# Kernel tuning notes

Hardware: AMD Instinct MI355X
Metric: run time of the kernel (lower is better)

The kernel has to match this reference:

```python
import jax, jax.numpy as jnp
import numpy as np

N_HEAD = 16
ROPE_BASE = 10000.0


def _rope_cos_sin(T, D, dtype):
    # D = head_size; matches RotaryEmbedding: emb = cat(freqs, freqs)
    inv_freq = 1.0 / (ROPE_BASE ** (jnp.arange(0, D, 2, dtype=jnp.float32) / D))
    t = jnp.arange(T, dtype=jnp.float32)
    freqs = t[:, None] * inv_freq[None, :]              # [T, D/2]
    emb = jnp.concatenate([freqs, freqs], axis=-1)      # [T, D]
    return jnp.cos(emb).astype(dtype), jnp.sin(emb).astype(dtype)


def _rotate_half(x):
    d = x.shape[-1] // 2
    return jnp.concatenate([-x[..., d:], x[..., :d]], axis=-1)


def setup_inputs() -> dict:
    key = jax.random.key(0)
    ks = jax.random.split(key, 5)
    B, T, C = 2, 2048, 1024
    s_in = 1.0 / np.sqrt(C)
    return {
        "x": jax.random.normal(ks[0], (B, T, C), dtype=jnp.float32),
        "w_attn": jax.random.normal(ks[1], (C, 3 * C), dtype=jnp.float32) * s_in,
        "b_attn": jnp.zeros((3 * C,), dtype=jnp.float32),
        "w_proj": jax.random.normal(ks[2], (C, C), dtype=jnp.float32) * s_in,
        "b_proj": jnp.zeros((C,), dtype=jnp.float32),
    }


def reference(x, w_attn, b_attn, w_proj, b_proj):
    B, T, C = x.shape
    H = N_HEAD
    D = C // H

    qkv = x @ w_attn + b_attn                            # [B,T,3C]
    q, k, v = jnp.split(qkv, 3, axis=-1)
    # [B,T,C] -> [B,H,T,D]
    to_heads = lambda a: a.reshape(B, T, H, D).transpose(0, 2, 1, 3)
    q, k, v = to_heads(q), to_heads(k), to_heads(v)

    cos, sin = _rope_cos_sin(T, D, x.dtype)              # [T,D] each, broadcast over B,H
    q = q * cos + _rotate_half(q) * sin
    k = k * cos + _rotate_half(k) * sin

    scale = 1.0 / np.sqrt(D)
    att = jnp.einsum("bhqd,bhkd->bhqk", q, k) * scale    # [B,H,T,T]
    causal = jnp.tril(jnp.ones((T, T), dtype=bool))
    att = jnp.where(causal, att, jnp.finfo(att.dtype).min)
    att = jax.nn.softmax(att, axis=-1)
    y = jnp.einsum("bhqk,bhkd->bhqd", att, v)            # [B,H,T,D]

    y = y.transpose(0, 2, 1, 3).reshape(B, T, C)
    return y @ w_proj + b_proj
```

## Files before the change

### kernel.cpp

```cpp
#include <hip/hip_runtime.h>
#include <hip/hip_bf16.h>

#define B_ 2
#define T_ 2048
#define C_ 1024
#define H_ 16
#define D_ 64

typedef __attribute__((ext_vector_type(8))) short bf16x8;
typedef __attribute__((ext_vector_type(4))) float f32x4;

static __device__ __forceinline__ float bf2f(unsigned short u) {
  union { unsigned int i; float f; } c;
  c.i = ((unsigned int)u) << 16;
  return c.f;
}
static __device__ __forceinline__ unsigned short f2bf(float f) {
  union { float f; unsigned int i; } c;
  c.f = f;
  unsigned int x = c.i;
  return (unsigned short)((x + 0x7fffu + ((x >> 16) & 1u)) >> 16);
}

static __device__ __forceinline__ void gl_lds16(const void* g, void* s) {
  __builtin_amdgcn_global_load_lds(
      (const __attribute__((address_space(1))) void*)g,
      (__attribute__((address_space(3))) void*)s, 16, 0, 0);
}

__global__ __launch_bounds__(256) void fill_kernel_f32(float* __restrict__ out,
                                                       int n, float v) {
  int i = blockIdx.x * 256 + threadIdx.x;
  if (i < n) out[i] = v;
}

__global__ __launch_bounds__(256) void cvt_bf16(const float* __restrict__ X,
                                                unsigned short* __restrict__ Xb) {
  int i = (blockIdx.x * 256 + threadIdx.x) * 8;
  float4 f0 = *(const float4*)(X + i);
  float4 f1 = *(const float4*)(X + i + 4);
  union { unsigned short u[8]; uint4 v; } p;
  p.u[0] = f2bf(f0.x); p.u[1] = f2bf(f0.y); p.u[2] = f2bf(f0.z); p.u[3] = f2bf(f0.w);
  p.u[4] = f2bf(f1.x); p.u[5] = f2bf(f1.y); p.u[6] = f2bf(f1.z); p.u[7] = f2bf(f1.w);
  *(uint4*)(Xb + i) = p.v;
}

__global__ __launch_bounds__(256) void transpose_cvt(const float* __restrict__ W,
                                                     unsigned short* __restrict__ WT,
                                                     int Kd, int Nd) {
  __shared__ float tile[32][33];
  const int n0 = blockIdx.x * 32, k0 = blockIdx.y * 32;
  const int tx = threadIdx.x & 31, ty = threadIdx.x >> 5;
#pragma unroll
  for (int i = 0; i < 4; ++i)
    tile[ty + i * 8][tx] = W[(size_t)(k0 + ty + i * 8) * Nd + n0 + tx];
  __syncthreads();
#pragma unroll
  for (int i = 0; i < 4; ++i)
    WT[(size_t)(n0 + ty + i * 8) * Kd + k0 + tx] = f2bf(tile[tx][ty + i * 8]);
}

__global__ __launch_bounds__(256) void v_transpose(const unsigned short* __restrict__ vP,
                                                   unsigned short* __restrict__ vT) {
  __shared__ unsigned short tile[64][72];
  const int t0 = blockIdx.x * 64;
  const int bh = blockIdx.y;
  const int b = bh >> 4;
  const int srow = threadIdx.x >> 3;
  const int sc8 = (threadIdx.x & 7) * 8;
#pragma unroll
  for (int it = 0; it < 2; ++it) {
    int r = srow + it * 32;
    *(uint4*)&tile[r][sc8] =
        *(const uint4*)(vP + (size_t)(b * T_ + t0 + r) * 1024 + (bh & 15) * 64 + sc8);
  }
  __syncthreads();
#pragma unroll
  for (int it = 0; it < 2; ++it) {
    int dd = srow + it * 32;
    union { unsigned short u[8]; uint4 v; } o;
#pragma unroll
    for (int j = 0; j < 8; ++j) o.u[j] = tile[sc8 + j][dd];
    *(uint4*)(vT + ((size_t)bh * 64 + dd) * 2048 + t0 + sc8) = o.v;
  }
}

template <int OUT_PLANES>
__global__ __launch_bounds__(256) void mfma_gemm(
    const unsigned short* __restrict__ A,
    const unsigned short* __restrict__ BT,
    const float* __restrict__ bias,
    unsigned short* __restrict__ qP, unsigned short* __restrict__ kP,
    unsigned short* __restrict__ vP, float* __restrict__ Fout,
    int N, int K) {
  __shared__ unsigned short As[128 * 64];
  __shared__ unsigned short Bs[128 * 64];

  const int tid = threadIdx.x;
  const int w = tid >> 6, lane = tid & 63;
  const int lo = lane & 15, g = lane >> 4;
  const int wm = (w >> 1) * 64, wn = (w & 1) * 64;
  const int m0 = blockIdx.y * 128, n0 = blockIdx.x * 128;

  const int lr8 = lane >> 3;

  const f32x4 zero4 = {0.f, 0.f, 0.f, 0.f};
  f32x4 acc[4][4] = {{zero4, zero4, zero4, zero4}, {zero4, zero4, zero4, zero4},
                     {zero4, zero4, zero4, zero4}, {zero4, zero4, zero4, zero4}};

  for (int k0 = 0; k0 < K; k0 += 64) {
    __syncthreads();
#pragma unroll
    for (int it = 0; it < 4; ++it) {
      const int base_row = w * 32 + it * 8;
      const int r = base_row + lr8;
      const int j = (lane & 7) ^ (r & 7);
      gl_lds16(A + (size_t)(m0 + r) * K + k0 + j * 8, &As[base_row * 64]);
      gl_lds16(BT + (size_t)(n0 + r) * K + k0 + j * 8, &Bs[base_row * 64]);
    }
    __syncthreads();

#pragma unroll
    for (int kk = 0; kk < 2; ++kk) {
      bf16x8 af[4], bfr[4];
#pragma unroll
      for (int i = 0; i < 4; ++i) {
        int ra = wm + i * 16 + lo;
        int rb = wn + i * 16 + lo;
        af[i]  = *(const bf16x8*)&As[ra * 64 + ((g + kk * 4) ^ (ra & 7)) * 8];
        bfr[i] = *(const bf16x8*)&Bs[rb * 64 + ((g + kk * 4) ^ (rb & 7)) * 8];
      }
#pragma unroll
      for (int i = 0; i < 4; ++i)
#pragma unroll
        for (int j = 0; j < 4; ++j)
          acc[i][j] = __builtin_amdgcn_mfma_f32_16x16x32_bf16(af[i], bfr[j],
                                                              acc[i][j], 0, 0, 0);
    }
  }

  float bv[4];
#pragma unroll
  for (int j = 0; j < 4; ++j) bv[j] = bias[n0 + wn + j * 16 + lo];

  if (OUT_PLANES) {
    const int pl = n0 >> 10;
    const int col0 = (n0 & 1023) + wn + lo;
    if (pl == 2) {
#pragma unroll
      for (int i = 0; i < 4; ++i)
#pragma unroll
        for (int r = 0; r < 4; ++r) {
          size_t row = (size_t)(m0 + wm + i * 16 + g * 4 + r);
#pragma unroll
          for (int j = 0; j < 4; ++j)
            vP[row * 1024 + col0 + j * 16] = f2bf(acc[i][j][r] + bv[j]);
        }
    } else {
      unsigned short* P = (pl == 0) ? qP : kP;
      const float scale = (pl == 0) ? 0.125f : 1.0f;
      const float invA = exp2f((float)(-2 * lo) * (13.287712379549449f / 64.0f)) *
                         0.15915494309189535f;
      const float invB = exp2f((float)(-2 * (lo + 16)) * (13.287712379549449f / 64.0f)) *
                         0.15915494309189535f;
#pragma unroll
      for (int i = 0; i < 4; ++i)
#pragma unroll
        for (int r = 0; r < 4; ++r) {
          const int row = m0 + wm + i * 16 + g * 4 + r;
          const float t = (float)(row & (T_ - 1));
          float ra = t * invA; ra -= floorf(ra);
          float rb = t * invB; rb -= floorf(rb);
          const float sA = __builtin_amdgcn_sinf(ra);
          const float cA = __builtin_amdgcn_cosf(ra);
          const float sB = __builtin_amdgcn_sinf(rb);
          const float cB = __builtin_amdgcn_cosf(rb);
          const float q1A = acc[i][0][r] + bv[0];
          const float q2A = acc[i][2][r] + bv[2];
          const float q1B = acc[i][1][r] + bv[1];
          const float q2B = acc[i][3][r] + bv[3];
          unsigned short* dst = P + (size_t)row * 1024 + col0;
          dst[0]  = f2bf((q1A * cA - q2A * sA) * scale);
          dst[32] = f2bf((q2A * cA + q1A * sA) * scale);
          dst[16] = f2bf((q1B * cB - q2B * sB) * scale);
          dst[48] = f2bf((q2B * cB + q1B * sB) * scale);
        }
    }
  } else {
#pragma unroll
    for (int i = 0; i < 4; ++i)
#pragma unroll
      for (int r = 0; r < 4; ++r) {
        size_t row = (size_t)(m0 + wm + i * 16 + g * 4 + r);
#pragma unroll
        for (int j = 0; j < 4; ++j)
          Fout[row * N + n0 + wn + j * 16 + lo] = acc[i][j][r] + bv[j];
      }
  }
}

__global__ __launch_bounds__(256) void flash_mfma6(
    unsigned short* __restrict__ qP,
    const unsigned short* __restrict__ kP,
    const unsigned short* __restrict__ vT) {
  const int bx = blockIdx.x;
  const int bh = blockIdx.y;
  const int b = bh >> 4, h = bh & 15;
  const int tid = threadIdx.x;
  const int w = tid >> 6, lane = tid & 63;
  const int lo = lane & 15, g = lane >> 4;

  __shared__ unsigned short Ks[64][72];
  __shared__ unsigned short VTs[64][72];
  __shared__ unsigned short Ps[64][72];

  const int srow = tid >> 3;
  const int sc8 = (tid & 7) * 8;
  const f32x4 zero4 = {0.f, 0.f, 0.f, 0.f};

#pragma unroll
  for (int half = 0; half < 2; ++half) {
    const int qt = half ? (31 - bx) : bx;
    const int rowq0 = b * T_ + qt * 64;

    const unsigned short* qrow = qP + (size_t)(rowq0 + w * 16 + lo) * 1024 + h * 64;
    bf16x8 aq0 = *(const bf16x8*)(qrow + g * 8);
    bf16x8 aq1 = *(const bf16x8*)(qrow + 32 + g * 8);

    f32x4 oacc[4] = {zero4, zero4, zero4, zero4};
    float lsum = 0.f;

    uint4 kreg0, kreg1, vreg0, vreg1;
    {
      const size_t kb = (size_t)(b * T_ + srow) * 1024 + h * 64 + sc8;
      kreg0 = *(const uint4*)(kP + kb);
      kreg1 = *(const uint4*)(kP + kb + (size_t)32 * 1024);
      const size_t vb = ((size_t)bh * 64 + srow) * 2048 + sc8;
      vreg0 = *(const uint4*)(vT + vb);
      vreg1 = *(const uint4*)(vT + vb + (size_t)32 * 2048);
    }

    for (int kt = 0; kt <= qt; ++kt) {
      __syncthreads();
      *(uint4*)&Ks[srow][sc8]       = kreg0;
      *(uint4*)&Ks[srow + 32][sc8]  = kreg1;
      *(uint4*)&VTs[srow][sc8]      = vreg0;
      *(uint4*)&VTs[srow + 32][sc8] = vreg1;
      __syncthreads();
      if (kt < qt) {
        const size_t kb = (size_t)(b * T_ + (kt + 1) * 64 + srow) * 1024 + h * 64 + sc8;
        kreg0 = *(const uint4*)(kP + kb);
        kreg1 = *(const uint4*)(kP + kb + (size_t)32 * 1024);
        const size_t vb = ((size_t)bh * 64 + srow) * 2048 + (kt + 1) * 64 + sc8;
        vreg0 = *(const uint4*)(vT + vb);
        vreg1 = *(const uint4*)(vT + vb + (size_t)32 * 2048);
      }

      f32x4 sacc[4] = {zero4, zero4, zero4, zero4};
      __builtin_amdgcn_s_setprio(1);
#pragma unroll
      for (int ct = 0; ct < 4; ++ct) {
        bf16x8 bk0 = *(const bf16x8*)&Ks[ct * 16 + lo][g * 8];
        bf16x8 bk1 = *(const bf16x8*)&Ks[ct * 16 + lo][32 + g * 8];
        sacc[ct] = __builtin_amdgcn_mfma_f32_16x16x32_bf16(bk0, aq0, sacc[ct], 0, 0, 0);
        sacc[ct] = __builtin_amdgcn_mfma_f32_16x16x32_bf16(bk1, aq1, sacc[ct], 0, 0, 0);
      }
      __builtin_amdgcn_s_setprio(0);

      if (kt == qt) {
#pragma unroll
        for (int ct = 0; ct < 4; ++ct)
#pragma unroll
          for (int r = 0; r < 4; ++r)
            if (ct * 16 + g * 4 + r > w * 16 + lo) sacc[ct][r] = -1e30f;
      }

#pragma unroll
      for (int ct = 0; ct < 4; ++ct) {
        float p0 = __expf(sacc[ct][0]);
        float p1 = __expf(sacc[ct][1]);
        float p2 = __expf(sacc[ct][2]);
        float p3 = __expf(sacc[ct][3]);
        lsum += (p0 + p1) + (p2 + p3);
        unsigned int u0 = (unsigned int)f2bf(p0) | ((unsigned int)f2bf(p1) << 16);
        unsigned int u1 = (unsigned int)f2bf(p2) | ((unsigned int)f2bf(p3) << 16);
        uint2 pw; pw.x = u0; pw.y = u1;
        *(uint2*)&Ps[w * 16 + lo][ct * 16 + g * 4] = pw;
      }

      bf16x8 ap0 = *(const bf16x8*)&Ps[w * 16 + lo][g * 8];
      bf16x8 ap1 = *(const bf16x8*)&Ps[w * 16 + lo][32 + g * 8];
      __builtin_amdgcn_s_setprio(1);
#pragma unroll
      for (int c2 = 0; c2 < 4; ++c2) {
        bf16x8 bv0 = *(const bf16x8*)&VTs[c2 * 16 + lo][g * 8];
        bf16x8 bv1 = *(const bf16x8*)&VTs[c2 * 16 + lo][32 + g * 8];
        oacc[c2] = __builtin_amdgcn_mfma_f32_16x16x32_bf16(ap0, bv0, oacc[c2], 0, 0, 0);
        oacc[c2] = __builtin_amdgcn_mfma_f32_16x16x32_bf16(ap1, bv1, oacc[c2], 0, 0, 0);
      }
      __builtin_amdgcn_s_setprio(0);
    }

    lsum += __shfl_xor(lsum, 16);
    lsum += __shfl_xor(lsum, 32);

#pragma unroll
    for (int r = 0; r < 4; ++r) {
      float inv_r = 1.0f / __shfl(lsum, g * 4 + r);
      unsigned short* dst = qP + (size_t)(rowq0 + w * 16 + g * 4 + r) * 1024 + h * 64 + lo;
#pragma unroll
      for (int c2 = 0; c2 < 4; ++c2)
        dst[c2 * 16] = f2bf(oacc[c2][r] * inv_r);
    }
  }
}

extern "C" void kernel_launch(void* const* d_in, const int* in_sizes, int n_in,
                              void* d_out, int out_size, void* d_ws, size_t ws_size,
                              hipStream_t stream) {
  const float *x = nullptr, *w_attn = nullptr, *b_attn = nullptr,
              *w_proj = nullptr, *b_proj = nullptr;
  for (int i = 0; i < n_in; ++i) {
    switch (in_sizes[i]) {
      case B_ * T_ * C_:  x      = (const float*)d_in[i]; break;
      case C_ * 3 * C_:   w_attn = (const float*)d_in[i]; break;
      case 3 * C_:        b_attn = (const float*)d_in[i]; break;
      case C_ * C_:       w_proj = (const float*)d_in[i]; break;
      case C_:            b_proj = (const float*)d_in[i]; break;
      default: break;
    }
  }
  float* out = (float*)d_out;
  const int nblk = (out_size + 255) / 256;

  if (!x || !w_attn || !b_attn || !w_proj || !b_proj) {
    fill_kernel_f32<<<nblk, 256, 0, stream>>>(out, out_size, 100.0f);
    return;
  }
  if (ws_size < (size_t)48 * 1024 * 1024) {
    fill_kernel_f32<<<nblk, 256, 0, stream>>>(out, out_size, 50.0f);
    return;
  }

  unsigned short* qP  = (unsigned short*)d_ws;
  unsigned short* kP  = qP + (size_t)(B_ * T_) * 1024;
  unsigned short* vP  = kP + (size_t)(B_ * T_) * 1024;
  unsigned short* vT  = vP + (size_t)(B_ * T_) * 1024;
  unsigned short* xb  = vT + (size_t)(B_ * T_) * 1024;
  unsigned short* waT = xb + (size_t)(B_ * T_) * C_;
  unsigned short* wpT = waT + (size_t)C_ * 3 * C_;

  transpose_cvt<<<dim3((3 * C_) / 32, C_ / 32), 256, 0, stream>>>(w_attn, waT, C_, 3 * C_);
  transpose_cvt<<<dim3(C_ / 32, C_ / 32), 256, 0, stream>>>(w_proj, wpT, C_, C_);
  cvt_bf16<<<(B_ * T_ * C_) / (256 * 8), 256, 0, stream>>>(x, xb);
  mfma_gemm<1><<<dim3((3 * C_) / 128, (B_ * T_) / 128), 256, 0, stream>>>(
      xb, waT, b_attn, qP, kP, vP, nullptr, 3 * C_, C_);
  v_transpose<<<dim3(T_ / 64, B_ * H_), 256, 0, stream>>>(vP, vT);
  flash_mfma6<<<dim3(16, B_ * H_), 256, 0, stream>>>(qP, kP, vT);
  mfma_gemm<0><<<dim3(C_ / 128, (B_ * T_) / 128), 256, 0, stream>>>(
      qP, wpT, b_proj, nullptr, nullptr, nullptr, out, C_, C_);
}
```

Before: 191.5 us.

## Merge prep kernels, stage GEMM epilogue through LDS, remap flash blocks to XCDs

Folds the two weight transpose-convert launches and the x conversion into one 3D-grid prep kernel to cut launch overhead. Both GEMM epilogues now write results into shared memory first, then store full rows with 16-byte vector writes, replacing scattered 2/4-byte global stores. The flash attention grid becomes 1D with a block-index remap so that the blocks of each batch-head group share an XCD, which should improve L2 reuse of K/V. These add extra barriers and LDS traffic in the epilogue and depend on the hardware assigning blocks to XCDs round-robin.

Measured after the change: 183.1 us. 1.05x faster.

```diff
diff --git a/kernel.cpp b/kernel.cpp
--- a/kernel.cpp
+++ b/kernel.cpp
@@ -34,21 +34,33 @@
   if (i < n) out[i] = v;
 }
 
-__global__ __launch_bounds__(256) void cvt_bf16(const float* __restrict__ X,
-                                                unsigned short* __restrict__ Xb) {
-  int i = (blockIdx.x * 256 + threadIdx.x) * 8;
-  float4 f0 = *(const float4*)(X + i);
-  float4 f1 = *(const float4*)(X + i + 4);
-  union { unsigned short u[8]; uint4 v; } p;
-  p.u[0] = f2bf(f0.x); p.u[1] = f2bf(f0.y); p.u[2] = f2bf(f0.z); p.u[3] = f2bf(f0.w);
-  p.u[4] = f2bf(f1.x); p.u[5] = f2bf(f1.y); p.u[6] = f2bf(f1.z); p.u[7] = f2bf(f1.w);
-  *(uint4*)(Xb + i) = p.v;
-}
-
-__global__ __launch_bounds__(256) void transpose_cvt(const float* __restrict__ W,
-                                                     unsigned short* __restrict__ WT,
-                                                     int Kd, int Nd) {
+__global__ __launch_bounds__(256) void prep_kernel(
+    const float* __restrict__ w_attn, const float* __restrict__ w_proj,
+    const float* __restrict__ x,
+    unsigned short* __restrict__ waT, unsigned short* __restrict__ wpT,
+    unsigned short* __restrict__ xb) {
   __shared__ float tile[32][33];
+  const int z = blockIdx.z;
+  if (z == 2) {
+    const int id = blockIdx.y * 96 + blockIdx.x;
+    if (id >= 2048) return;
+    int i = (id * 256 + threadIdx.x) * 8;
+    float4 f0 = *(const float4*)(x + i);
+    float4 f1 = *(const float4*)(x + i + 4);
+    union { unsigned short u[8]; uint4 v; } p;
+    p.u[0] = f2bf(f0.x); p.u[1] = f2bf(f0.y); p.u[2] = f2bf(f0.z); p.u[3] = f2bf(f0.w);
+    p.u[4] = f2bf(f1.x); p.u[5] = f2bf(f1.y); p.u[6] = f2bf(f1.z); p.u[7] = f2bf(f1.w);
+    *(uint4*)(xb + i) = p.v;
+    return;
+  }
+  const float* W;
+  unsigned short* WT;
+  int Kd, Nd;
+  if (z == 0) { W = w_attn; WT = waT; Kd = 1024; Nd = 3072; }
+  else {
+    if (blockIdx.x >= 32) return;
+    W = w_proj; WT = wpT; Kd = 1024; Nd = 1024;
+  }
   const int n0 = blockIdx.x * 32, k0 = blockIdx.y * 32;
   const int tx = threadIdx.x & 31, ty = threadIdx.x >> 5;
 #pragma unroll
@@ -93,8 +105,9 @@
     unsigned short* __restrict__ qP, unsigned short* __restrict__ kP,
     unsigned short* __restrict__ vP, float* __restrict__ Fout,
     int N, int K) {
-  __shared__ unsigned short As[128 * 64];
-  __shared__ unsigned short Bs[128 * 64];
+  __shared__ unsigned short S[128 * 128];
+  unsigned short* As = S;
+  unsigned short* Bs = S + 128 * 64;
 
   const int tid = threadIdx.x;
   const int w = tid >> 6, lane = tid & 63;
@@ -145,30 +158,30 @@
 
   if (OUT_PLANES) {
     const int pl = n0 >> 10;
-    const int col0 = (n0 & 1023) + wn + lo;
+    __syncthreads();
     if (pl == 2) {
 #pragma unroll
       for (int i = 0; i < 4; ++i)
 #pragma unroll
         for (int r = 0; r < 4; ++r) {
-          size_t row = (size_t)(m0 + wm + i * 16 + g * 4 + r);
+          const int row = wm + i * 16 + g * 4 + r;
 #pragma unroll
           for (int j = 0; j < 4; ++j)
-            vP[row * 1024 + col0 + j * 16] = f2bf(acc[i][j][r] + bv[j]);
+            S[row * 128 + wn + j * 16 + lo] = f2bf(acc[i][j][r] + bv[j]);
         }
     } else {
-      unsigned short* P = (pl == 0) ? qP : kP;
       const float scale = (pl == 0) ? 0.125f : 1.0f;
       const float invA = exp2f((float)(-2 * lo) * (13.287712379549449f / 64.0f)) *
                          0.15915494309189535f;
       const float invB = exp2f((float)(-2 * (lo + 16)) * (13.287712379549449f / 64.0f)) *
                          0.15915494309189535f;
+      const int c0 = wn + lo;
 #pragma unroll
       for (int i = 0; i < 4; ++i)
 #pragma unroll
         for (int r = 0; r < 4; ++r) {
-          const int row = m0 + wm + i * 16 + g * 4 + r;
-          const float t = (float)(row & (T_ - 1));
+          const int row = wm + i * 16 + g * 4 + r;
+          const float t = (float)((m0 + row) & (T_ - 1));
           float ra = t * invA; ra -= floorf(ra);
           float rb = t * invB; rb -= floorf(rb);
           const float sA = __builtin_amdgcn_sinf(ra);
@@ -179,23 +192,49 @@
           const float q2A = acc[i][2][r] + bv[2];
           const float q1B = acc[i][1][r] + bv[1];
           const float q2B = acc[i][3][r] + bv[3];
-          unsigned short* dst = P + (size_t)row * 1024 + col0;
-          dst[0]  = f2bf((q1A * cA - q2A * sA) * scale);
-          dst[32] = f2bf((q2A * cA + q1A * sA) * scale);
-          dst[16] = f2bf((q1B * cB - q2B * sB) * scale);
-          dst[48] = f2bf((q2B * cB + q1B * sB) * scale);
+          S[row * 128 + c0]      = f2bf((q1A * cA - q2A * sA) * scale);
+          S[row * 128 + c0 + 32] = f2bf((q2A * cA + q1A * sA) * scale);
+          S[row * 128 + c0 + 16] = f2bf((q1B * cB - q2B * sB) * scale);
+          S[row * 128 + c0 + 48] = f2bf((q2B * cB + q1B * sB) * scale);
         }
     }
+    __syncthreads();
+    unsigned short* P = (pl == 0) ? qP : (pl == 1) ? kP : vP;
+    const int pcol0 = n0 & 1023;
+#pragma unroll
+    for (int it2 = 0; it2 < 8; ++it2) {
+      const int p = it2 * 256 + tid;
+      const int lrow = p >> 4;
+      const int lcol = (p & 15) * 8;
+      uint4 v4 = *(const uint4*)&S[lrow * 128 + lcol];
+      *(uint4*)(P + (size_t)(m0 + lrow) * 1024 + pcol0 + lcol) = v4;
+    }
   } else {
-#pragma unroll
-    for (int i = 0; i < 4; ++i)
-#pragma unroll
-      for (int r = 0; r < 4; ++r) {
-        size_t row = (size_t)(m0 + wm + i * 16 + g * 4 + r);
-#pragma unroll
-        for (int j = 0; j < 4; ++j)
-          Fout[row * N + n0 + wn + j * 16 + lo] = acc[i][j][r] + bv[j];
-      }
+    float* Sf = (float*)S;
+#pragma unroll
+    for (int hh = 0; hh < 2; ++hh) {
+      __syncthreads();
+      if ((w >> 1) == hh) {
+#pragma unroll
+        for (int i = 0; i < 4; ++i)
+#pragma unroll
+          for (int r = 0; r < 4; ++r) {
+            const int lrow = i * 16 + g * 4 + r;
+#pragma unroll
+            for (int j = 0; j < 4; ++j)
+              Sf[lrow * 128 + wn + j * 16 + lo] = acc[i][j][r] + bv[j];
+          }
+      }
+      __syncthreads();
+#pragma unroll
+      for (int it2 = 0; it2 < 8; ++it2) {
+        const int p = it2 * 256 + tid;
+        const int lrow = p >> 5;
+        const int lcol = (p & 31) * 4;
+        float4 v4 = *(const float4*)&Sf[lrow * 128 + lcol];
+        *(float4*)(Fout + (size_t)(m0 + hh * 64 + lrow) * N + n0 + lcol) = v4;
+      }
+    }
   }
 }
 
@@ -203,8 +242,11 @@
     unsigned short* __restrict__ qP,
     const unsigned short* __restrict__ kP,
     const unsigned short* __restrict__ vT) {
-  const int bx = blockIdx.x;
-  const int bh = blockIdx.y;
+  const int cid = blockIdx.x;
+  const int xcd = cid & 7;
+  const int k6 = cid >> 3;
+  const int bh = xcd * 4 + (k6 >> 4);
+  const int bx = k6 & 15;
   const int b = bh >> 4, h = bh & 15;
   const int tid = threadIdx.x;
   const int w = tid >> 6, lane = tid & 63;
@@ -350,13 +392,11 @@
   unsigned short* waT = xb + (size_t)(B_ * T_) * C_;
   unsigned short* wpT = waT + (size_t)C_ * 3 * C_;
 
-  transpose_cvt<<<dim3((3 * C_) / 32, C_ / 32), 256, 0, stream>>>(w_attn, waT, C_, 3 * C_);
-  transpose_cvt<<<dim3(C_ / 32, C_ / 32), 256, 0, stream>>>(w_proj, wpT, C_, C_);
-  cvt_bf16<<<(B_ * T_ * C_) / (256 * 8), 256, 0, stream>>>(x, xb);
+  prep_kernel<<<dim3(96, 32, 3), 256, 0, stream>>>(w_attn, w_proj, x, waT, wpT, xb);
   mfma_gemm<1><<<dim3((3 * C_) / 128, (B_ * T_) / 128), 256, 0, stream>>>(
       xb, waT, b_attn, qP, kP, vP, nullptr, 3 * C_, C_);
   v_transpose<<<dim3(T_ / 64, B_ * H_), 256, 0, stream>>>(vP, vT);
-  flash_mfma6<<<dim3(16, B_ * H_), 256, 0, stream>>>(qP, kP, vT);
+  flash_mfma6<<<dim3(512), 256, 0, stream>>>(qP, kP, vT);
   mfma_gemm<0><<<dim3(C_ / 128, (B_ * T_) / 128), 256, 0, stream>>>(
       qP, wpT, b_proj, nullptr, nullptr, nullptr, out, C_, C_);
 }
```
